# Kernel optimization log

Hardware: AMD Instinct MI355X
Metric: run time of the kernel (lower is better)

The kernel has to match this reference:

```python
import jax, jax.numpy as jnp
import numpy as np

H = 8          # n_heads
D = 1024       # dim_tgt == dim_mem
DQ = D // H    # per-head dim = 128
BN = 512       # LFFN bottleneck (hardcoded in module)
HID = 1024     # LFFN hidden (hardcoded in module)
B = 16
S_T = 1024     # target length
S_M = 2048     # memory length
SCALE = DQ ** 0.25  # module uses dim_q ** (1/4)
EPS = 1e-5


def _ln(x, g, b):
    m = jnp.mean(x, axis=-1, keepdims=True)
    v = jnp.mean(jnp.square(x - m), axis=-1, keepdims=True)
    return (x - m) * jax.lax.rsqrt(v + EPS) * g + b


def _mhla(xq, xk, xv, Wq, Wk, Wv, Wo, masked):
    # per-head projections: x [b,s,D] x W [H,D,DQ] -> [b,H,s,DQ]
    Q = jnp.einsum('bsq,hqd->bhsd', xq, Wq)
    K = jnp.einsum('bsq,hqd->bhsd', xk, Wk)
    V = jnp.einsum('bsq,hqd->bhsd', xv, Wv)
    if masked:
        s, d = Q.shape[-2], Q.shape[-1]
        # module adds log(triu(ones).T) directly to Q: 0 where d_idx<=t, -inf otherwise
        m = jnp.where(jnp.arange(d)[None, :] <= jnp.arange(s)[:, None], 0.0, -jnp.inf)
        Q = Q + m.astype(Q.dtype)
    # softmax_col(K^T/d_k) over head-dim axis == softmax(K/d_k, axis=-1)
    A = jnp.einsum('bhsd,bhse->bhde', jax.nn.softmax(K / SCALE, axis=-1), V)  # [b,H,DQ,DQ]
    Bm = jnp.einsum('bhsd,bhde->bhse', jax.nn.softmax(Q / SCALE, axis=-1), A)  # [b,H,s,DQ]
    b, h, w, dd = Bm.shape
    # torch .view(b, w, h*d) on contiguous [b,h,w,d]: raw row-major reshape (no transpose)
    Bm = Bm.reshape(b, w, h * dd)
    return Bm @ Wo.T


def setup_inputs():
    key = jax.random.key(0)
    ks = jax.random.split(key, 24)
    r = lambda k, sh, s=0.02: (jax.random.normal(k, sh, jnp.float32) * s)
    return {
        'mem': jax.random.normal(ks[0], (B, S_M, D), jnp.float32),
        'y': jax.random.normal(ks[1], (B, S_T, D), jnp.float32),
        # self-attention (masked)
        'Wq1': r(ks[2], (H, D, DQ)), 'Wk1': r(ks[3], (H, D, DQ)), 'Wv1': r(ks[4], (H, D, DQ)),
        'Wo1': r(ks[5], (D, D)),
        # cross-attention with memory
        'Wq2': r(ks[6], (H, D, DQ)), 'Wk2': r(ks[7], (H, D, DQ)), 'Wv2': r(ks[8], (H, D, DQ)),
        'Wo2': r(ks[9], (D, D)),
        # LFFN (torch Linear weights are [out, in])
        'E1': r(ks[10], (BN, D)), 'D1': r(ks[11], (HID, BN)),
        'E2': r(ks[12], (BN, HID)), 'D2': r(ks[13], (D, BN)),
        # LayerNorm affine params
        'g1': jnp.ones((D,), jnp.float32), 'b1': jnp.zeros((D,), jnp.float32),
        'g2': jnp.ones((D,), jnp.float32), 'b2': jnp.zeros((D,), jnp.float32),
        'g3': jnp.ones((D,), jnp.float32), 'b3': jnp.zeros((D,), jnp.float32),
    }


def reference(mem, y, Wq1, Wk1, Wv1, Wo1, Wq2, Wk2, Wv2, Wo2,
              E1, D1, E2, D2, g1, b1, g2, b2, g3, b3):
    # dropout layers are identity in eval mode
    y = y + _mhla(y, y, y, Wq1, Wk1, Wv1, Wo1, masked=True)
    y = _ln(y, g1, b1)
    y = y + _mhla(y, mem, mem, Wq2, Wk2, Wv2, Wo2, masked=False)
    y = _ln(y, g2, b2)
    # LFFN: E1 -> D1 -> swish -> E2 -> D2
    h = (y @ E1.T) @ D1.T
    h = h * jax.nn.sigmoid(h)
    ffn = (h @ E2.T) @ D2.T
    y = _ln(y + ffn, g3, b3)
    return y
```

## Files before the change

### kernel.cpp

```cpp
#include <hip/hip_runtime.h>
#include <hip/hip_bf16.h>

#define DEVI __device__ __forceinline__

typedef __bf16 bfrag __attribute__((ext_vector_type(8)));
typedef unsigned short us8 __attribute__((ext_vector_type(8)));
typedef float f32x4 __attribute__((ext_vector_type(4)));
typedef unsigned short ushort_t;

static constexpr int NB  = 16;
static constexpr int NH  = 8;
static constexpr int DIM = 1024;
static constexpr int DQh = 128;
static constexpr int ST  = 1024;
static constexpr int SM  = 2048;
static constexpr float INV_SCALE = 0.29730177875068026f;
static constexpr float LN_EPS = 1e-5f;

DEVI ushort_t f2bf(float f) {
  __hip_bfloat16 h = __float2bfloat16(f);
  return __builtin_bit_cast(ushort_t, h);
}
DEVI float bf2f(ushort_t u) {
  return __bfloat162float(__builtin_bit_cast(__hip_bfloat16, u));
}
DEVI bfrag ldfrag(const ushort_t* p) {
  return __builtin_bit_cast(bfrag, *(const us8*)p);
}
DEVI void gl16(const ushort_t* g, ushort_t* l) {
  __builtin_amdgcn_global_load_lds(
      (const __attribute__((address_space(1))) void*)g,
      (__attribute__((address_space(3))) void*)l, 16, 0, 0);
}

enum { ST_BF16 = 0, ST_SWISH = 1, ST_F32RES = 2 };

__global__ __launch_bounds__(256, 4)
void gemm_qkv(const ushort_t* __restrict__ A, const ushort_t* __restrict__ Bt,
              ushort_t* __restrict__ P0, ushort_t* __restrict__ P1,
              int M, int N, int K, int logS, int smflags)
{
  __shared__ ushort_t As[128][32];
  __shared__ ushort_t Bs[128][32];
  const int tid = threadIdx.x;
  int bx = blockIdx.x, by = blockIdx.y;
  {
    const int gx = gridDim.x;
    const int nwg = gx * gridDim.y;
    int bid = by * gx + bx;
    if ((nwg & 7) == 0) bid = (bid & 7) * (nwg >> 3) + (bid >> 3);
    bx = bid % gx; by = bid / gx;
  }
  const int m0 = by * 128, n0 = bx * 128;

  const int lane = tid & 63;
  const int w = tid >> 6;
  const int wr = w * 32;
  const int frow = lane & 15;
  const int q = lane >> 4;

  const int grow = lane >> 2;
  const int gk = ((lane & 3) ^ ((lane >> 3) & 3)) * 8;
  const ushort_t* Ag = A + (long)(m0 + w * 32 + grow) * K + gk;
  const ushort_t* Bg = Bt + (long)(n0 + w * 32 + grow) * K + gk;

  f32x4 acc[2][8];
  #pragma unroll
  for (int i = 0; i < 2; ++i)
    #pragma unroll
    for (int j = 0; j < 8; ++j) acc[i][j] = f32x4{0.f, 0.f, 0.f, 0.f};

  const int kqs = (frow >> 1) & 3;
  for (int k0 = 0; k0 < K; k0 += 32) {
    __syncthreads();
    gl16(Ag + k0,                &As[w * 32][0]);
    gl16(Ag + k0 + (long)16 * K, &As[w * 32 + 16][0]);
    gl16(Bg + k0,                &Bs[w * 32][0]);
    gl16(Bg + k0 + (long)16 * K, &Bs[w * 32 + 16][0]);
    __syncthreads();
    const int kq = (q ^ kqs) * 8;
    const bfrag af0 = ldfrag(&As[wr + frow][kq]);
    const bfrag af1 = ldfrag(&As[wr + 16 + frow][kq]);
    #pragma unroll
    for (int j = 0; j < 8; ++j) {
      const bfrag bf = ldfrag(&Bs[j * 16 + frow][kq]);
      acc[0][j] = __builtin_amdgcn_mfma_f32_16x16x32_bf16(af0, bf, acc[0][j], 0, 0, 0);
      acc[1][j] = __builtin_amdgcn_mfma_f32_16x16x32_bf16(af1, bf, acc[1][j], 0, 0, 0);
    }
  }

  const int sel = n0 >> 10;
  const bool dosm = (smflags >> sel) & 1;
  const int h = (n0 >> 7) & 7;
  ushort_t* __restrict__ Bq = (sel == 0) ? P0 : P1;
  const int S = 1 << logS;
  const int b_blk = m0 >> logS;
  const int s_m0 = m0 & (S - 1);

  if (dosm) {
    #pragma unroll
    for (int i = 0; i < 2; ++i) {
      #pragma unroll
      for (int e = 0; e < 4; ++e) {
        float v[8];
        #pragma unroll
        for (int j = 0; j < 8; ++j) v[j] = acc[i][j][e] * INV_SCALE;
        float mx = v[0];
        #pragma unroll
        for (int j = 1; j < 8; ++j) mx = fmaxf(mx, v[j]);
        mx = fmaxf(mx, __shfl_xor(mx, 1));
        mx = fmaxf(mx, __shfl_xor(mx, 2));
        mx = fmaxf(mx, __shfl_xor(mx, 4));
        mx = fmaxf(mx, __shfl_xor(mx, 8));
        float sm = 0.f;
        #pragma unroll
        for (int j = 0; j < 8; ++j) { v[j] = __expf(v[j] - mx); sm += v[j]; }
        sm += __shfl_xor(sm, 1);
        sm += __shfl_xor(sm, 2);
        sm += __shfl_xor(sm, 4);
        sm += __shfl_xor(sm, 8);
        const float inv = 1.0f / sm;
        #pragma unroll
        for (int j = 0; j < 8; ++j) acc[i][j][e] = v[j] * inv;
      }
    }
  }

  ushort_t* zbase = Bq + (long)(h * 16 + b_blk) * S * 128;
  #pragma unroll
  for (int i = 0; i < 2; ++i) {
    const int sb = s_m0 + wr + i * 16 + q * 4;
    ushort_t* rowb = zbase + (long)(sb >> 3) * 1024 + (sb & 7);
    #pragma unroll
    for (int j = 0; j < 8; ++j) {
      ushort4 o = make_ushort4(f2bf(acc[i][j][0]), f2bf(acc[i][j][1]),
                               f2bf(acc[i][j][2]), f2bf(acc[i][j][3]));
      *(ushort4*)(rowb + (j * 16 + frow) * 8) = o;
    }
  }
}

template<bool MASKED>
__global__ __launch_bounds__(256, 3)
void fused_qa(const ushort_t* __restrict__ A, const ushort_t* __restrict__ Wq,
              const ushort_t* __restrict__ AT, ushort_t* __restrict__ Out)
{
  __shared__ ushort_t As[128][32];
  __shared__ ushort_t Bs[128][32];
  __shared__ ushort_t Ps[4][32][128];
  const int tid = threadIdx.x;
  int h = blockIdx.x, by = blockIdx.y;
  {
    const int gx = gridDim.x;
    const int nwg = gx * gridDim.y;
    int bid = by * gx + h;
    if ((nwg & 7) == 0) bid = (bid & 7) * (nwg >> 3) + (bid >> 3);
    h = bid % gx; by = bid / gx;
  }
  const int m0 = by * 128;

  const int lane = tid & 63;
  const int w = tid >> 6;
  const int wr = w * 32;
  const int frow = lane & 15;
  const int q = lane >> 4;

  const int grow = lane >> 2;
  const int gk = ((lane & 3) ^ ((lane >> 3) & 3)) * 8;
  const ushort_t* Ag = A + (long)(m0 + w * 32 + grow) * 1024 + gk;
  const ushort_t* Bg = Wq + (long)(h * 128 + w * 32 + grow) * 1024 + gk;

  f32x4 acc[2][8];
  #pragma unroll
  for (int i = 0; i < 2; ++i)
    #pragma unroll
    for (int j = 0; j < 8; ++j) acc[i][j] = f32x4{0.f, 0.f, 0.f, 0.f};

  const int kqs = (frow >> 1) & 3;
  for (int k0 = 0; k0 < 1024; k0 += 32) {
    __syncthreads();
    gl16(Ag + k0,             &As[w * 32][0]);
    gl16(Ag + k0 + 16 * 1024, &As[w * 32 + 16][0]);
    gl16(Bg + k0,             &Bs[w * 32][0]);
    gl16(Bg + k0 + 16 * 1024, &Bs[w * 32 + 16][0]);
    __syncthreads();
    const int kq = (q ^ kqs) * 8;
    const bfrag af0 = ldfrag(&As[wr + frow][kq]);
    const bfrag af1 = ldfrag(&As[wr + 16 + frow][kq]);
    #pragma unroll
    for (int j = 0; j < 8; ++j) {
      const bfrag bf = ldfrag(&Bs[j * 16 + frow][kq]);
      acc[0][j] = __builtin_amdgcn_mfma_f32_16x16x32_bf16(af0, bf, acc[0][j], 0, 0, 0);
      acc[1][j] = __builtin_amdgcn_mfma_f32_16x16x32_bf16(af1, bf, acc[1][j], 0, 0, 0);
    }
  }

  #pragma unroll
  for (int i = 0; i < 2; ++i) {
    #pragma unroll
    for (int e = 0; e < 4; ++e) {
      const int row32 = i * 16 + q * 4 + e;
      const int srow = (m0 + wr + row32) & (ST - 1);
      float v[8];
      #pragma unroll
      for (int j = 0; j < 8; ++j) {
        v[j] = acc[i][j][e] * INV_SCALE;
        if (MASKED && (j * 16 + frow) > srow) v[j] = -3.0e38f;
      }
      float mx = v[0];
      #pragma unroll
      for (int j = 1; j < 8; ++j) mx = fmaxf(mx, v[j]);
      mx = fmaxf(mx, __shfl_xor(mx, 1));
      mx = fmaxf(mx, __shfl_xor(mx, 2));
      mx = fmaxf(mx, __shfl_xor(mx, 4));
      mx = fmaxf(mx, __shfl_xor(mx, 8));
      float sm = 0.f;
      #pragma unroll
      for (int j = 0; j < 8; ++j) { v[j] = __expf(v[j] - mx); sm += v[j]; }
      sm += __shfl_xor(sm, 1);
      sm += __shfl_xor(sm, 2);
      sm += __shfl_xor(sm, 4);
      sm += __shfl_xor(sm, 8);
      const float inv = 1.0f / sm;
      const int sw = (row32 >> 1) & 3;
      ushort_t* pr = &Ps[w][row32][0];
      #pragma unroll
      for (int j = 0; j < 8; ++j) {
        const int c = j * 16 + frow;
        const int pos = (c & ~31) | ((((c >> 3) & 3) ^ sw) << 3) | (c & 7);
        pr[pos] = f2bf(v[j] * inv);
      }
    }
  }

  f32x4 acc2[2][8];
  #pragma unroll
  for (int i = 0; i < 2; ++i)
    #pragma unroll
    for (int j = 0; j < 8; ++j) acc2[i][j] = f32x4{0.f, 0.f, 0.f, 0.f};

  const ushort_t* Atg = AT + (long)((h << 4) + (m0 >> 10)) * 16384 +
                        (long)(w * 32 + grow) * 128 + gk;
  for (int d0 = 0; d0 < 128; d0 += 32) {
    __syncthreads();
    gl16(Atg + d0,            &Bs[w * 32][0]);
    gl16(Atg + d0 + 16 * 128, &Bs[w * 32 + 16][0]);
    __syncthreads();
    const int kq = (q ^ kqs) * 8;
    const bfrag af0 = ldfrag(&Ps[w][frow][d0 + kq]);
    const bfrag af1 = ldfrag(&Ps[w][16 + frow][d0 + kq]);
    #pragma unroll
    for (int j = 0; j < 8; ++j) {
      const bfrag bf = ldfrag(&Bs[j * 16 + frow][kq]);
      acc2[0][j] = __builtin_amdgcn_mfma_f32_16x16x32_bf16(af0, bf, acc2[0][j], 0, 0, 0);
      acc2[1][j] = __builtin_amdgcn_mfma_f32_16x16x32_bf16(af1, bf, acc2[1][j], 0, 0, 0);
    }
  }

  ushort_t* ob = Out + (long)(m0 >> 10) * (ST * DIM);
  #pragma unroll
  for (int i = 0; i < 2; ++i) {
    #pragma unroll
    for (int e = 0; e < 4; ++e) {
      const int srow = (m0 + wr + i * 16 + q * 4 + e) & (ST - 1);
      ushort_t* orow = ob + (long)(h * 128 + (srow >> 3)) * DIM + (srow & 7) * 128;
      #pragma unroll
      for (int j = 0; j < 8; ++j)
        orow[j * 16 + frow] = f2bf(acc2[i][j][e]);
    }
  }
}

template<int STORE>
__global__ __launch_bounds__(256, 2)
void gemm_bb(const ushort_t* __restrict__ A, const ushort_t* __restrict__ Bt,
             const float* __restrict__ Res,
             ushort_t* __restrict__ P0, float* __restrict__ Cf,
             int M, int N, int K)
{
  __shared__ ushort_t As[128][32];
  __shared__ ushort_t Bs[128][32];
  const int tid = threadIdx.x;
  int bx = blockIdx.x, by = blockIdx.y;
  {
    const int gx = gridDim.x;
    const int nwg = gx * gridDim.y;
    int bid = by * gx + bx;
    if ((nwg & 7) == 0) bid = (bid & 7) * (nwg >> 3) + (bid >> 3);
    bx = bid % gx; by = bid / gx;
  }
  const int m0 = by * 128, n0 = bx * 128;

  const int lane = tid & 63;
  const int w = tid >> 6;
  const int wr = (w >> 1) * 64, wc = (w & 1) * 64;
  const int frow = lane & 15;
  const int q = lane >> 4;

  const int grow = lane >> 2;
  const int gk = ((lane & 3) ^ ((lane >> 3) & 3)) * 8;
  const ushort_t* Ag = A + (long)(m0 + w * 32 + grow) * K + gk;
  const ushort_t* Bg = Bt + (long)(n0 + w * 32 + grow) * K + gk;

  f32x4 acc[4][4];
  #pragma unroll
  for (int i = 0; i < 4; ++i)
    #pragma unroll
    for (int j = 0; j < 4; ++j) acc[i][j] = f32x4{0.f, 0.f, 0.f, 0.f};

  const int kqs = (frow >> 1) & 3;
  for (int k0 = 0; k0 < K; k0 += 32) {
    __syncthreads();
    gl16(Ag + k0,                &As[w * 32][0]);
    gl16(Ag + k0 + (long)16 * K, &As[w * 32 + 16][0]);
    gl16(Bg + k0,                &Bs[w * 32][0]);
    gl16(Bg + k0 + (long)16 * K, &Bs[w * 32 + 16][0]);
    __syncthreads();
    const int kq = (q ^ kqs) * 8;
    bfrag af[4], bf[4];
    #pragma unroll
    for (int i = 0; i < 4; ++i) af[i] = ldfrag(&As[wr + i * 16 + frow][kq]);
    #pragma unroll
    for (int j = 0; j < 4; ++j) bf[j] = ldfrag(&Bs[wc + j * 16 + frow][kq]);
    #pragma unroll
    for (int i = 0; i < 4; ++i)
      #pragma unroll
      for (int j = 0; j < 4; ++j)
        acc[i][j] = __builtin_amdgcn_mfma_f32_16x16x32_bf16(af[i], bf[j], acc[i][j], 0, 0, 0);
  }

  const int rb = q * 4;
  #pragma unroll
  for (int i = 0; i < 4; ++i) {
    #pragma unroll
    for (int j = 0; j < 4; ++j) {
      #pragma unroll
      for (int e = 0; e < 4; ++e) {
        const int gm = m0 + wr + i * 16 + rb + e;
        const int gn = n0 + wc + j * 16 + frow;
        float val = acc[i][j][e];
        if constexpr (STORE == ST_SWISH) val = val / (1.0f + __expf(-val));
        if constexpr (STORE == ST_F32RES) {
          Cf[(long)gm * N + gn] = val + Res[(long)gm * N + gn];
        } else {
          P0[(long)gm * N + gn] = f2bf(val);
        }
      }
    }
  }
}

__global__ __launch_bounds__(256, 2)
void gemm_ktv(const ushort_t* __restrict__ Kp, const ushort_t* __restrict__ Vp,
              float* __restrict__ P, int S, int SC)
{
  __shared__ ushort_t As[4096];
  __shared__ ushort_t Bs[4096];
  const int tid = threadIdx.x;
  const int z = blockIdx.x;
  const int ch = blockIdx.y;
  const int lane = tid & 63, w = tid >> 6;
  const int wr = (w >> 1) * 64, wc = (w & 1) * 64;
  const int frow = lane & 15, q = lane >> 4;
  const long zoff = (long)z * S * 128 + ((long)(ch * SC) >> 3) * 1024;
  const ushort_t* Vg = Vp + zoff + lane * 8;
  const ushort_t* Kg = Kp + zoff + lane * 8;

  f32x4 acc[4][4];
  #pragma unroll
  for (int i = 0; i < 4; ++i)
    #pragma unroll
    for (int j = 0; j < 4; ++j) acc[i][j] = f32x4{0.f, 0.f, 0.f, 0.f};

  for (int s0 = 0; s0 < SC; s0 += 32) {
    const long go = ((long)s0 >> 3) * 1024;
    __syncthreads();
    gl16(Vg + go + (2 * w) * 512,     &As[(2 * w) * 512]);
    gl16(Vg + go + (2 * w + 1) * 512, &As[(2 * w + 1) * 512]);
    gl16(Kg + go + (2 * w) * 512,     &Bs[(2 * w) * 512]);
    gl16(Kg + go + (2 * w + 1) * 512, &Bs[(2 * w + 1) * 512]);
    __syncthreads();
    bfrag af[4], bf[4];
    #pragma unroll
    for (int i = 0; i < 4; ++i)
      af[i] = ldfrag(&As[q * 1024 + (wr + i * 16 + frow) * 8]);
    #pragma unroll
    for (int j = 0; j < 4; ++j)
      bf[j] = ldfrag(&Bs[q * 1024 + (wc + j * 16 + frow) * 8]);
    #pragma unroll
    for (int i = 0; i < 4; ++i)
      #pragma unroll
      for (int j = 0; j < 4; ++j)
        acc[i][j] = __builtin_amdgcn_mfma_f32_16x16x32_bf16(af[i], bf[j], acc[i][j], 0, 0, 0);
  }
  float* Pz = P + ((long)ch * 128 + z) * 16384;
  const int rb = q * 4;
  #pragma unroll
  for (int i = 0; i < 4; ++i)
    #pragma unroll
    for (int j = 0; j < 4; ++j)
      #pragma unroll
      for (int e = 0; e < 4; ++e)
        Pz[(long)(wr + i * 16 + rb + e) * 128 + (wc + j * 16 + frow)] = acc[i][j][e];
}

__global__ __launch_bounds__(256)
void ktv_reduce(const float* __restrict__ P, ushort_t* __restrict__ AT, int nch)
{
  const long i = ((long)blockIdx.x * 256 + threadIdx.x) * 4;
  float4 s = *(const float4*)(P + i);
  for (int c = 1; c < nch; ++c) {
    const float4 v = *(const float4*)(P + (long)c * 2097152 + i);
    s.x += v.x; s.y += v.y; s.z += v.z; s.w += v.w;
  }
  ushort4 o = make_ushort4(f2bf(s.x), f2bf(s.y), f2bf(s.z), f2bf(s.w));
  *(ushort4*)(AT + i) = o;
}

__global__ __launch_bounds__(256)
void layernorm_k(const float* __restrict__ X, const float* __restrict__ G,
                 const float* __restrict__ Bta, float* __restrict__ Y,
                 ushort_t* __restrict__ Yb)
{
  const int row = blockIdx.x;
  const int t = threadIdx.x;
  const float4 v = *(const float4*)(X + (long)row * DIM + t * 4);
  float s  = v.x + v.y + v.z + v.w;
  float sq = v.x * v.x + v.y * v.y + v.z * v.z + v.w * v.w;
  #pragma unroll
  for (int o = 32; o; o >>= 1) { s += __shfl_xor(s, o); sq += __shfl_xor(sq, o); }
  __shared__ float ps[4], pq[4];
  if ((t & 63) == 0) { ps[t >> 6] = s; pq[t >> 6] = sq; }
  __syncthreads();
  s  = ps[0] + ps[1] + ps[2] + ps[3];
  sq = pq[0] + pq[1] + pq[2] + pq[3];
  const float mean = s * (1.0f / DIM);
  const float var  = sq * (1.0f / DIM) - mean * mean;
  const float rstd = rsqrtf(var + LN_EPS);
  const float4 gv = *(const float4*)(G + t * 4);
  const float4 bv = *(const float4*)(Bta + t * 4);
  float4 o;
  o.x = (v.x - mean) * rstd * gv.x + bv.x;
  o.y = (v.y - mean) * rstd * gv.y + bv.y;
  o.z = (v.z - mean) * rstd * gv.z + bv.z;
  o.w = (v.w - mean) * rstd * gv.w + bv.w;
  *(float4*)(Y + (long)row * DIM + t * 4) = o;
  if (Yb) {
    ushort4 ob = make_ushort4(f2bf(o.x), f2bf(o.y), f2bf(o.z), f2bf(o.w));
    *(ushort4*)(Yb + (long)row * DIM + t * 4) = ob;
  }
}

__global__ __launch_bounds__(256)
void transpose_cast(const float* __restrict__ W, ushort_t* __restrict__ Wt)
{
  __shared__ float tile[32][33];
  const int z = blockIdx.z;
  const int kb = blockIdx.y * 32;
  const int nb = blockIdx.x * 32;
  const float* src = W + (long)z * DIM * DQh;
  ushort_t* dst = Wt + (long)z * DIM * DQh;
  const int tx = threadIdx.x & 31;
  const int ty = threadIdx.x >> 5;
  #pragma unroll
  for (int r = 0; r < 32; r += 8)
    tile[ty + r][tx] = src[(long)(kb + ty + r) * DQh + nb + tx];
  __syncthreads();
  #pragma unroll
  for (int r = 0; r < 32; r += 8)
    dst[(long)(nb + ty + r) * DIM + kb + tx] = f2bf(tile[tx][ty + r]);
}

__global__ __launch_bounds__(256)
void cast_bf16(const float* __restrict__ X, ushort_t* __restrict__ Yq)
{
  const long i = ((long)blockIdx.x * 256 + threadIdx.x) * 4;
  const float4 v = *(const float4*)(X + i);
  ushort4 sv = make_ushort4(f2bf(v.x), f2bf(v.y), f2bf(v.z), f2bf(v.w));
  *(ushort4*)(Yq + i) = sv;
}


extern "C" void kernel_launch(void* const* d_in, const int* in_sizes, int n_in,
                              void* d_out, int out_size, void* d_ws, size_t ws_size,
                              hipStream_t stream)
{
  (void)in_sizes; (void)n_in; (void)out_size; (void)ws_size;
  const float* mem = (const float*)d_in[0];
  const float* y0  = (const float*)d_in[1];
  const float* Wq1 = (const float*)d_in[2];
  const float* Wk1 = (const float*)d_in[3];
  const float* Wv1 = (const float*)d_in[4];
  const float* Wo1 = (const float*)d_in[5];
  const float* Wq2 = (const float*)d_in[6];
  const float* Wk2 = (const float*)d_in[7];
  const float* Wv2 = (const float*)d_in[8];
  const float* Wo2 = (const float*)d_in[9];
  const float* E1  = (const float*)d_in[10];
  const float* D1  = (const float*)d_in[11];
  const float* E2  = (const float*)d_in[12];
  const float* D2  = (const float*)d_in[13];
  const float* g1  = (const float*)d_in[14];
  const float* b1  = (const float*)d_in[15];
  const float* g2  = (const float*)d_in[16];
  const float* b2  = (const float*)d_in[17];
  const float* g3  = (const float*)d_in[18];
  const float* b3  = (const float*)d_in[19];

  char* ws = (char*)d_ws;
  const size_t MB = 1ull << 20;
  ushort_t* wkv1  = (ushort_t*)(ws + 0 * MB);
  ushort_t* wq1t  = (ushort_t*)(ws + 4 * MB);
  ushort_t* wkv2  = (ushort_t*)(ws + 6 * MB);
  ushort_t* wq2t  = (ushort_t*)(ws + 10 * MB);
  ushort_t* wo1b  = (ushort_t*)(ws + 12 * MB);
  ushort_t* wo2b  = (ushort_t*)(ws + 14 * MB);
  ushort_t* e1b   = (ushort_t*)(ws + 16 * MB);
  ushort_t* d1b   = (ushort_t*)(ws + 17 * MB);
  ushort_t* e2b   = (ushort_t*)(ws + 18 * MB);
  ushort_t* d2b   = (ushort_t*)(ws + 19 * MB);
  ushort_t* y0b   = (ushort_t*)(ws + 20 * MB);
  ushort_t* memb  = (ushort_t*)(ws + 52 * MB);
  ushort_t* bn2   = (ushort_t*)(ws + 116 * MB);
  ushort_t* kbuf  = (ushort_t*)(ws + 148 * MB);
  ushort_t* vbuf  = (ushort_t*)(ws + 212 * MB);
  ushort_t* amatT = (ushort_t*)(ws + 276 * MB);
  ushort_t* attnb = (ushort_t*)(ws + 280 * MB);
  float*    ybuf  = (float*)(ws + 312 * MB);
  ushort_t* ybf   = (ushort_t*)(ws + 376 * MB);
  ushort_t* hbuf  = (ushort_t*)(ws + 408 * MB);
  float*    pbuf  = (float*)(ws + 440 * MB);
  ushort_t* bn1   = attnb;

  cast_bf16<<<16384, 256, 0, stream>>>(y0, y0b);
  cast_bf16<<<32768, 256, 0, stream>>>(mem, memb);
  transpose_cast<<<dim3(4, 32, 8), 256, 0, stream>>>(Wk1, wkv1);
  transpose_cast<<<dim3(4, 32, 8), 256, 0, stream>>>(Wv1, wkv1 + (1 << 20));
  transpose_cast<<<dim3(4, 32, 8), 256, 0, stream>>>(Wq1, wq1t);
  transpose_cast<<<dim3(4, 32, 8), 256, 0, stream>>>(Wk2, wkv2);
  transpose_cast<<<dim3(4, 32, 8), 256, 0, stream>>>(Wv2, wkv2 + (1 << 20));
  transpose_cast<<<dim3(4, 32, 8), 256, 0, stream>>>(Wq2, wq2t);
  cast_bf16<<<1024, 256, 0, stream>>>(Wo1, wo1b);
  cast_bf16<<<1024, 256, 0, stream>>>(Wo2, wo2b);
  cast_bf16<<<512, 256, 0, stream>>>(E1, e1b);
  cast_bf16<<<512, 256, 0, stream>>>(D1, d1b);
  cast_bf16<<<512, 256, 0, stream>>>(E2, e2b);
  cast_bf16<<<512, 256, 0, stream>>>(D2, d2b);

  gemm_qkv<<<dim3(16, 128), 256, 0, stream>>>(
      y0b, wkv1, kbuf, vbuf, NB * ST, 2048, DIM, 10,  0b01);
  gemm_ktv<<<dim3(128, 2), 256, 0, stream>>>(kbuf, vbuf, pbuf, ST, 512);
  ktv_reduce<<<2048, 256, 0, stream>>>(pbuf, amatT, 2);
  fused_qa<true><<<dim3(8, 128), 256, 0, stream>>>(y0b, wq1t, amatT, attnb);
  gemm_bb<ST_F32RES><<<dim3(8, 128), 256, 0, stream>>>(
      attnb, wo1b, y0, nullptr, ybuf, NB * ST, DIM, DIM);
  layernorm_k<<<NB * ST, 256, 0, stream>>>(ybuf, g1, b1, ybuf, ybf);

  gemm_qkv<<<dim3(16, 256), 256, 0, stream>>>(
      memb, wkv2, kbuf, vbuf, NB * SM, 2048, DIM, 11, 0b01);
  gemm_ktv<<<dim3(128, 4), 256, 0, stream>>>(kbuf, vbuf, pbuf, SM, 512);
  ktv_reduce<<<2048, 256, 0, stream>>>(pbuf, amatT, 4);
  fused_qa<false><<<dim3(8, 128), 256, 0, stream>>>(ybf, wq2t, amatT, attnb);
  gemm_bb<ST_F32RES><<<dim3(8, 128), 256, 0, stream>>>(
      attnb, wo2b, ybuf, nullptr, ybuf, NB * ST, DIM, DIM);
  layernorm_k<<<NB * ST, 256, 0, stream>>>(ybuf, g2, b2, ybuf, ybf);

  gemm_bb<ST_BF16><<<dim3(4, 128), 256, 0, stream>>>(
      ybf, e1b, nullptr, bn1, nullptr, NB * ST, 512, DIM);
  gemm_bb<ST_SWISH><<<dim3(8, 128), 256, 0, stream>>>(
      bn1, d1b, nullptr, hbuf, nullptr, NB * ST, DIM, 512);
  gemm_bb<ST_BF16><<<dim3(4, 128), 256, 0, stream>>>(
      hbuf, e2b, nullptr, bn2, nullptr, NB * ST, 512, DIM);
  gemm_bb<ST_F32RES><<<dim3(8, 128), 256, 0, stream>>>(
      bn2, d2b, ybuf, nullptr, ybuf, NB * ST, DIM, 512);
  layernorm_k<<<NB * ST, 256, 0, stream>>>(ybuf, g3, b3, (float*)d_out, nullptr);
}
```

Before: 844.7 us.

## Fold LayerNorm 1 and 2 into adjacent GEMM epilogues via stat partials and weight absorption

Removes the first two standalone LayerNorm passes. The residual GEMMs now emit the pre-norm activations in fp32 and bf16, plus per-row partial sums and sums of squares, and a small kernel reduces these to mean and rstd. The consumers apply the normalization inside their epilogues: gamma is folded into the Wq2 and E1 weights, and the mean and beta terms enter as precomputed column vectors. This saves full read/write passes over the activations, but feeds the GEMMs unnormalized bf16 inputs, which risks precision loss, and computes variance as E[x²]−μ², which can cancel badly.

```diff
diff --git a/kernel.cpp b/kernel.cpp
--- a/kernel.cpp
+++ b/kernel.cpp
@@ -33,7 +33,8 @@
       (__attribute__((address_space(3))) void*)l, 16, 0, 0);
 }
 
-enum { ST_BF16 = 0, ST_SWISH = 1, ST_F32RES = 2 };
+enum { ST_BF16 = 0, ST_SWISH = 1, ST_ABS = 2, ST_YSTAT = 3, ST_ZSTAT = 4,
+       ST_ZRES = 5 };
 
 __global__ __launch_bounds__(256, 4)
 void gemm_qkv(const ushort_t* __restrict__ A, const ushort_t* __restrict__ Bt,
@@ -140,10 +141,12 @@
   }
 }
 
-template<bool MASKED>
+template<bool MASKED, bool ABSORB>
 __global__ __launch_bounds__(256, 3)
 void fused_qa(const ushort_t* __restrict__ A, const ushort_t* __restrict__ Wq,
-              const ushort_t* __restrict__ AT, ushort_t* __restrict__ Out)
+              const ushort_t* __restrict__ AT, ushort_t* __restrict__ Out,
+              const float* __restrict__ SIn, const float* __restrict__ C1,
+              const float* __restrict__ C2)
 {
   __shared__ ushort_t As[128][32];
   __shared__ ushort_t Bs[128][32];
@@ -195,16 +198,34 @@
     }
   }
 
+  float c1j[8], c2j[8];
+  if (ABSORB) {
+    #pragma unroll
+    for (int j = 0; j < 8; ++j) {
+      c1j[j] = C1[h * 128 + j * 16 + frow];
+      c2j[j] = C2[h * 128 + j * 16 + frow];
+    }
+  }
+
   #pragma unroll
   for (int i = 0; i < 2; ++i) {
     #pragma unroll
     for (int e = 0; e < 4; ++e) {
       const int row32 = i * 16 + q * 4 + e;
-      const int srow = (m0 + wr + row32) & (ST - 1);
+      const int gmr = m0 + wr + row32;
+      const int srow = gmr & (ST - 1);
       float v[8];
       #pragma unroll
+      for (int j = 0; j < 8; ++j) v[j] = acc[i][j][e];
+      if (ABSORB) {
+        const float mu = SIn[gmr * 2], rr = SIn[gmr * 2 + 1];
+        #pragma unroll
+        for (int j = 0; j < 8; ++j)
+          v[j] = rr * v[j] - rr * mu * c1j[j] + c2j[j];
+      }
+      #pragma unroll
       for (int j = 0; j < 8; ++j) {
-        v[j] = acc[i][j][e] * INV_SCALE;
+        v[j] *= INV_SCALE;
         if (MASKED && (j * 16 + frow) > srow) v[j] = -3.0e38f;
       }
       float mx = v[0];
@@ -274,9 +295,11 @@
 template<int STORE>
 __global__ __launch_bounds__(256, 2)
 void gemm_bb(const ushort_t* __restrict__ A, const ushort_t* __restrict__ Bt,
-             const float* __restrict__ Res,
-             ushort_t* __restrict__ P0, float* __restrict__ Cf,
-             int M, int N, int K)
+             const float* __restrict__ Res, const float* __restrict__ SIn,
+             const float* __restrict__ Gv, const float* __restrict__ Bv,
+             const float* __restrict__ C1, const float* __restrict__ C2,
+             ushort_t* __restrict__ Pb, float* __restrict__ Cf,
+             float* __restrict__ PStat, int M, int N, int K)
 {
   __shared__ ushort_t As[128][32];
   __shared__ ushort_t Bs[128][32];
@@ -330,24 +353,140 @@
   }
 
   const int rb = q * 4;
-  #pragma unroll
-  for (int i = 0; i < 4; ++i) {
-    #pragma unroll
-    for (int j = 0; j < 4; ++j) {
+  if constexpr (STORE == ST_YSTAT || STORE == ST_ZSTAT) {
+    float gvj[4], bvj[4];
+    if constexpr (STORE == ST_ZSTAT) {
+      #pragma unroll
+      for (int j = 0; j < 4; ++j) {
+        gvj[j] = Gv[n0 + wc + j * 16 + frow];
+        bvj[j] = Bv[n0 + wc + j * 16 + frow];
+      }
+    }
+    #pragma unroll
+    for (int i = 0; i < 4; ++i) {
       #pragma unroll
       for (int e = 0; e < 4; ++e) {
         const int gm = m0 + wr + i * 16 + rb + e;
-        const int gn = n0 + wc + j * 16 + frow;
-        float val = acc[i][j][e];
-        if constexpr (STORE == ST_SWISH) val = val / (1.0f + __expf(-val));
-        if constexpr (STORE == ST_F32RES) {
-          Cf[(long)gm * N + gn] = val + Res[(long)gm * N + gn];
-        } else {
-          P0[(long)gm * N + gn] = f2bf(val);
+        float mu = 0.f, rr = 0.f;
+        if constexpr (STORE == ST_ZSTAT) { mu = SIn[gm * 2]; rr = SIn[gm * 2 + 1]; }
+        float s = 0.f, sq = 0.f, vals[4];
+        #pragma unroll
+        for (int j = 0; j < 4; ++j) {
+          const int gn = n0 + wc + j * 16 + frow;
+          float rv = Res[(long)gm * N + gn];
+          if constexpr (STORE == ST_ZSTAT) rv = (rv - mu) * rr * gvj[j] + bvj[j];
+          const float v = acc[i][j][e] + rv;
+          vals[j] = v; s += v; sq += v * v;
         }
-      }
-    }
-  }
+        #pragma unroll
+        for (int j = 0; j < 4; ++j) {
+          const int gn = n0 + wc + j * 16 + frow;
+          Cf[(long)gm * N + gn] = vals[j];
+          Pb[(long)gm * N + gn] = f2bf(vals[j]);
+        }
+        s += __shfl_xor(s, 1);  sq += __shfl_xor(sq, 1);
+        s += __shfl_xor(s, 2);  sq += __shfl_xor(sq, 2);
+        s += __shfl_xor(s, 4);  sq += __shfl_xor(sq, 4);
+        s += __shfl_xor(s, 8);  sq += __shfl_xor(sq, 8);
+        if (frow == 0) {
+          const int p = (n0 >> 7) * 2 + (wc >> 6);
+          PStat[((long)gm * 16 + p) * 2]     = s;
+          PStat[((long)gm * 16 + p) * 2 + 1] = sq;
+        }
+      }
+    }
+  } else if constexpr (STORE == ST_ABS) {
+    float c1j[4], c2j[4];
+    #pragma unroll
+    for (int j = 0; j < 4; ++j) {
+      c1j[j] = C1[n0 + wc + j * 16 + frow];
+      c2j[j] = C2[n0 + wc + j * 16 + frow];
+    }
+    #pragma unroll
+    for (int i = 0; i < 4; ++i) {
+      #pragma unroll
+      for (int e = 0; e < 4; ++e) {
+        const int gm = m0 + wr + i * 16 + rb + e;
+        const float mu = SIn[gm * 2], rr = SIn[gm * 2 + 1];
+        #pragma unroll
+        for (int j = 0; j < 4; ++j) {
+          const int gn = n0 + wc + j * 16 + frow;
+          const float v = rr * acc[i][j][e] - rr * mu * c1j[j] + c2j[j];
+          Pb[(long)gm * N + gn] = f2bf(v);
+        }
+      }
+    }
+  } else if constexpr (STORE == ST_ZRES) {
+    float gvj[4], bvj[4];
+    #pragma unroll
+    for (int j = 0; j < 4; ++j) {
+      gvj[j] = Gv[n0 + wc + j * 16 + frow];
+      bvj[j] = Bv[n0 + wc + j * 16 + frow];
+    }
+    #pragma unroll
+    for (int i = 0; i < 4; ++i) {
+      #pragma unroll
+      for (int e = 0; e < 4; ++e) {
+        const int gm = m0 + wr + i * 16 + rb + e;
+        const float mu = SIn[gm * 2], rr = SIn[gm * 2 + 1];
+        #pragma unroll
+        for (int j = 0; j < 4; ++j) {
+          const int gn = n0 + wc + j * 16 + frow;
+          const float rv = Res[(long)gm * N + gn];
+          const float z = (rv - mu) * rr * gvj[j] + bvj[j];
+          Cf[(long)gm * N + gn] = acc[i][j][e] + z;
+        }
+      }
+    }
+  } else {
+    #pragma unroll
+    for (int i = 0; i < 4; ++i) {
+      #pragma unroll
+      for (int j = 0; j < 4; ++j) {
+        #pragma unroll
+        for (int e = 0; e < 4; ++e) {
+          const int gm = m0 + wr + i * 16 + rb + e;
+          const int gn = n0 + wc + j * 16 + frow;
+          float val = acc[i][j][e];
+          if constexpr (STORE == ST_SWISH) val = val / (1.0f + __expf(-val));
+          Pb[(long)gm * N + gn] = f2bf(val);
+        }
+      }
+    }
+  }
+}
+
+__global__ __launch_bounds__(256)
+void stats_reduce(const float* __restrict__ PS, float* __restrict__ SO)
+{
+  const int row = blockIdx.x * 256 + threadIdx.x;
+  float s = 0.f, sq = 0.f;
+  const float* p = PS + (long)row * 32;
+  #pragma unroll
+  for (int k = 0; k < 16; ++k) { s += p[2 * k]; sq += p[2 * k + 1]; }
+  const float mu = s * (1.0f / 1024.0f);
+  const float var = sq * (1.0f / 1024.0f) - mu * mu;
+  SO[row * 2] = mu;
+  SO[row * 2 + 1] = rsqrtf(var + LN_EPS);
+}
+
+__global__ __launch_bounds__(256)
+void cvec(const float* __restrict__ W, const float* __restrict__ g,
+          const float* __restrict__ b, float* __restrict__ c1,
+          float* __restrict__ c2, int hstride, int nb_h, int nstride,
+          int kstride, int K)
+{
+  const int n = (blockIdx.x * 256 + threadIdx.x) >> 6;
+  const int lane = threadIdx.x & 63;
+  const long base = (long)(n / nb_h) * hstride + (long)(n % nb_h) * nstride;
+  float s1 = 0.f, s2 = 0.f;
+  for (int k = lane; k < K; k += 64) {
+    const float wv = W[base + (long)k * kstride];
+    s1 += g[k] * wv; s2 += b[k] * wv;
+  }
+  #pragma unroll
+  for (int o = 32; o; o >>= 1) { s1 += __shfl_xor(s1, o); s2 += __shfl_xor(s2, o); }
+  if (lane == 0) { c1[n] = s1; c2[n] = s2; }
 }
 
 __global__ __launch_bounds__(256, 2)
@@ -419,8 +558,7 @@
 
 __global__ __launch_bounds__(256)
 void layernorm_k(const float* __restrict__ X, const float* __restrict__ G,
-                 const float* __restrict__ Bta, float* __restrict__ Y,
-                 ushort_t* __restrict__ Yb)
+                 const float* __restrict__ Bta, float* __restrict__ Y)
 {
   const int row = blockIdx.x;
   const int t = threadIdx.x;
@@ -445,14 +583,12 @@
   o.z = (v.z - mean) * rstd * gv.z + bv.z;
   o.w = (v.w - mean) * rstd * gv.w + bv.w;
   *(float4*)(Y + (long)row * DIM + t * 4) = o;
-  if (Yb) {
-    ushort4 ob = make_ushort4(f2bf(o.x), f2bf(o.y), f2bf(o.z), f2bf(o.w));
-    *(ushort4*)(Yb + (long)row * DIM + t * 4) = ob;
-  }
-}
-
+}
+
+template<bool SCALE>
 __global__ __launch_bounds__(256)
-void transpose_cast(const float* __restrict__ W, ushort_t* __restrict__ Wt)
+void transpose_cast(const float* __restrict__ W, const float* __restrict__ g,
+                    ushort_t* __restrict__ Wt)
 {
   __shared__ float tile[32][33];
   const int z = blockIdx.z;
@@ -466,9 +602,10 @@
   for (int r = 0; r < 32; r += 8)
     tile[ty + r][tx] = src[(long)(kb + ty + r) * DQh + nb + tx];
   __syncthreads();
+  const float gs = SCALE ? g[kb + tx] : 1.0f;
   #pragma unroll
   for (int r = 0; r < 32; r += 8)
-    dst[(long)(nb + ty + r) * DIM + kb + tx] = f2bf(tile[tx][ty + r]);
+    dst[(long)(nb + ty + r) * DIM + kb + tx] = f2bf(tile[tx][ty + r] * gs);
 }
 
 __global__ __launch_bounds__(256)
@@ -477,6 +614,19 @@
   const long i = ((long)blockIdx.x * 256 + threadIdx.x) * 4;
   const float4 v = *(const float4*)(X + i);
   ushort4 sv = make_ushort4(f2bf(v.x), f2bf(v.y), f2bf(v.z), f2bf(v.w));
+  *(ushort4*)(Yq + i) = sv;
+}
+
+__global__ __launch_bounds__(256)
+void cast_scale(const float* __restrict__ X, const float* __restrict__ g,
+                ushort_t* __restrict__ Yq)
+{
+  const long i = ((long)blockIdx.x * 256 + threadIdx.x) * 4;
+  const int k = (int)(i & 1023);
+  const float4 v = *(const float4*)(X + i);
+  const float4 gv = *(const float4*)(g + k);
+  ushort4 sv = make_ushort4(f2bf(v.x * gv.x), f2bf(v.y * gv.y),
+                            f2bf(v.z * gv.z), f2bf(v.w * gv.w));
   *(ushort4*)(Yq + i) = sv;
 }
 
@@ -522,6 +672,14 @@
   ushort_t* y0b   = (ushort_t*)(ws + 20 * MB);
   ushort_t* memb  = (ushort_t*)(ws + 52 * MB);
   ushort_t* bn2   = (ushort_t*)(ws + 116 * MB);
+  float*    pstat1 = (float*)(ws + 132 * MB);
+  float*    pstat2 = (float*)(ws + 134 * MB);
+  float*    stats1 = (float*)(ws + 136 * MB);
+  float*    stats2 = (float*)(ws + 137 * MB);
+  float*    c1q    = (float*)(ws + 138 * MB);
+  float*    c2q    = (float*)(ws + 139 * MB);
+  float*    c1e    = (float*)(ws + 140 * MB);
+  float*    c2e    = (float*)(ws + 141 * MB);
   ushort_t* kbuf  = (ushort_t*)(ws + 148 * MB);
   ushort_t* vbuf  = (ushort_t*)(ws + 212 * MB);
   ushort_t* amatT = (ushort_t*)(ws + 276 * MB);
@@ -534,44 +692,54 @@
 
   cast_bf16<<<16384, 256, 0, stream>>>(y0, y0b);
   cast_bf16<<<32768, 256, 0, stream>>>(mem, memb);
-  transpose_cast<<<dim3(4, 32, 8), 256, 0, stream>>>(Wk1, wkv1);
-  transpose_cast<<<dim3(4, 32, 8), 256, 0, stream>>>(Wv1, wkv1 + (1 << 20));
-  transpose_cast<<<dim3(4, 32, 8), 256, 0, stream>>>(Wq1, wq1t);
-  transpose_cast<<<dim3(4, 32, 8), 256, 0, stream>>>(Wk2, wkv2);
-  transpose_cast<<<dim3(4, 32, 8), 256, 0, stream>>>(Wv2, wkv2 + (1 << 20));
-  transpose_cast<<<dim3(4, 32, 8), 256, 0, stream>>>(Wq2, wq2t);
+  transpose_cast<false><<<dim3(4, 32, 8), 256, 0, stream>>>(Wk1, nullptr, wkv1);
+  transpose_cast<false><<<dim3(4, 32, 8), 256, 0, stream>>>(Wv1, nullptr, wkv1 + (1 << 20));
+  transpose_cast<false><<<dim3(4, 32, 8), 256, 0, stream>>>(Wq1, nullptr, wq1t);
+  transpose_cast<false><<<dim3(4, 32, 8), 256, 0, stream>>>(Wk2, nullptr, wkv2);
+  transpose_cast<false><<<dim3(4, 32, 8), 256, 0, stream>>>(Wv2, nullptr, wkv2 + (1 << 20));
+  transpose_cast<true><<<dim3(4, 32, 8), 256, 0, stream>>>(Wq2, g1, wq2t);
   cast_bf16<<<1024, 256, 0, stream>>>(Wo1, wo1b);
   cast_bf16<<<1024, 256, 0, stream>>>(Wo2, wo2b);
-  cast_bf16<<<512, 256, 0, stream>>>(E1, e1b);
+  cast_scale<<<512, 256, 0, stream>>>(E1, g2, e1b);
   cast_bf16<<<512, 256, 0, stream>>>(D1, d1b);
   cast_bf16<<<512, 256, 0, stream>>>(E2, e2b);
   cast_bf16<<<512, 256, 0, stream>>>(D2, d2b);
+  cvec<<<256, 256, 0, stream>>>(Wq2, g1, b1, c1q, c2q, DIM * DQh, 128, 1, 128, 1024);
+  cvec<<<128, 256, 0, stream>>>(E1, g2, b2, c1e, c2e, 0, 512, 1024, 1, 1024);
 
   gemm_qkv<<<dim3(16, 128), 256, 0, stream>>>(
-      y0b, wkv1, kbuf, vbuf, NB * ST, 2048, DIM, 10,  0b01);
+      y0b, wkv1, kbuf, vbuf, NB * ST, 2048, DIM, 10, 0b01);
   gemm_ktv<<<dim3(128, 2), 256, 0, stream>>>(kbuf, vbuf, pbuf, ST, 512);
   ktv_reduce<<<2048, 256, 0, stream>>>(pbuf, amatT, 2);
-  fused_qa<true><<<dim3(8, 128), 256, 0, stream>>>(y0b, wq1t, amatT, attnb);
-  gemm_bb<ST_F32RES><<<dim3(8, 128), 256, 0, stream>>>(
-      attnb, wo1b, y0, nullptr, ybuf, NB * ST, DIM, DIM);
-  layernorm_k<<<NB * ST, 256, 0, stream>>>(ybuf, g1, b1, ybuf, ybf);
+  fused_qa<true, false><<<dim3(8, 128), 256, 0, stream>>>(
+      y0b, wq1t, amatT, attnb, nullptr, nullptr, nullptr);
+  gemm_bb<ST_YSTAT><<<dim3(8, 128), 256, 0, stream>>>(
+      attnb, wo1b, y0, nullptr, nullptr, nullptr, nullptr, nullptr,
+      ybf, ybuf, pstat1, NB * ST, DIM, DIM);
+  stats_reduce<<<64, 256, 0, stream>>>(pstat1, stats1);
 
   gemm_qkv<<<dim3(16, 256), 256, 0, stream>>>(
       memb, wkv2, kbuf, vbuf, NB * SM, 2048, DIM, 11, 0b01);
   gemm_ktv<<<dim3(128, 4), 256, 0, stream>>>(kbuf, vbuf, pbuf, SM, 512);
   ktv_reduce<<<2048, 256, 0, stream>>>(pbuf, amatT, 4);
-  fused_qa<false><<<dim3(8, 128), 256, 0, stream>>>(ybf, wq2t, amatT, attnb);
-  gemm_bb<ST_F32RES><<<dim3(8, 128), 256, 0, stream>>>(
-      attnb, wo2b, ybuf, nullptr, ybuf, NB * ST, DIM, DIM);
-  layernorm_k<<<NB * ST, 256, 0, stream>>>(ybuf, g2, b2, ybuf, ybf);
-
+  fused_qa<false, true><<<dim3(8, 128), 256, 0, stream>>>(
+      ybf, wq2t, amatT, attnb, stats1, c1q, c2q);
+  gemm_bb<ST_ZSTAT><<<dim3(8, 128), 256, 0, stream>>>(
+      attnb, wo2b, ybuf, stats1, g1, b1, nullptr, nullptr,
+      ybf, ybuf, pstat2, NB * ST, DIM, DIM);
+  stats_reduce<<<64, 256, 0, stream>>>(pstat2, stats2);
+
+  gemm_bb<ST_ABS><<<dim3(4, 128), 256, 0, stream>>>(
+      ybf, e1b, nullptr, stats2, nullptr, nullptr, c1e, c2e,
+      bn1, nullptr, nullptr, NB * ST, 512, DIM);
+  gemm_bb<ST_SWISH><<<dim3(8, 128), 256, 0, stream>>>(
+      bn1, d1b, nullptr, nullptr, nullptr, nullptr, nullptr, nullptr,
+      hbuf, nullptr, nullptr, NB * ST, DIM, 512);
   gemm_bb<ST_BF16><<<dim3(4, 128), 256, 0, stream>>>(
-      ybf, e1b, nullptr, bn1, nullptr, NB * ST, 512, DIM);
-  gemm_bb<ST_SWISH><<<dim3(8, 128), 256, 0, stream>>>(
-      bn1, d1b, nullptr, hbuf, nullptr, NB * ST, DIM, 512);
-  gemm_bb<ST_BF16><<<dim3(4, 128), 256, 0, stream>>>(
-      hbuf, e2b, nullptr, bn2, nullptr, NB * ST, 512, DIM);
-  gemm_bb<ST_F32RES><<<dim3(8, 128), 256, 0, stream>>>(
-      bn2, d2b, ybuf, nullptr, ybuf, NB * ST, DIM, 512);
-  layernorm_k<<<NB * ST, 256, 0, stream>>>(ybuf, g3, b3, (float*)d_out, nullptr);
-}
+      hbuf, e2b, nullptr, nullptr, nullptr, nullptr, nullptr, nullptr,
+      bn2, nullptr, nullptr, NB * ST, 512, DIM);
+  gemm_bb<ST_ZRES><<<dim3(8, 128), 256, 0, stream>>>(
+      bn2, d2b, ybuf, stats2, g2, b2, nullptr, nullptr,
+      nullptr, ybuf, nullptr, NB * ST, DIM, 512);
+  layernorm_k<<<NB * ST, 256, 0, stream>>>(ybuf, g3, b3, (float*)d_out);
+}
```

Result: no change. 845.6 us (+0.1%).
